# Kernel tuning notes

Hardware: AMD Instinct MI355X
Metric: run time of the kernel (lower is better)

Reference implementation:

```python
import jax, jax.numpy as jnp
import numpy as np

NUM_HEADS = 4
HIDDEN = 128
LN_EPS = 1e-6
NEG_INF = -1e9


def setup_inputs() -> dict:
    key = jax.random.key(0)
    ks = jax.random.split(key, 8)
    B, S, H, NH = 64, 512, HIDDEN, NUM_HEADS
    enc = jax.random.normal(ks[0], (B, S, H), dtype=jnp.float32)
    mask = jax.random.randint(ks[1], (B, 1, S, S), 0, 2, dtype=jnp.int32)
    scale = 1.0 / np.sqrt(H)
    # torch Linear(H, H*NH, bias=False): weight is (H*NH, H); store transposed (H, H*NH)
    Wq = jax.random.normal(ks[2], (H, H * NH), dtype=jnp.float32) * scale
    Wk = jax.random.normal(ks[3], (H, H * NH), dtype=jnp.float32) * scale
    Wv = jax.random.normal(ks[4], (H, H * NH), dtype=jnp.float32) * scale
    Wo = jax.random.normal(ks[5], (H * NH, H), dtype=jnp.float32) * (1.0 / np.sqrt(H * NH))
    gamma = jnp.ones((H,), dtype=jnp.float32)
    beta = jnp.zeros((H,), dtype=jnp.float32)
    return {"enc": enc, "mask": mask, "Wq": Wq, "Wk": Wk, "Wv": Wv, "Wo": Wo, "gamma": gamma, "beta": beta}


def reference(enc, mask, Wq, Wk, Wv, Wo, gamma, beta):
    B, S, H = enc.shape
    NH = NUM_HEADS
    # projections -> (B, NH, S, H): each head has head_dim == hidden_units
    Q = (enc @ Wq).reshape(B, S, NH, H).transpose(0, 2, 1, 3)
    K = (enc @ Wk).reshape(B, S, NH, H).transpose(0, 2, 1, 3)
    V = (enc @ Wv).reshape(B, S, NH, H).transpose(0, 2, 1, 3)
    # scaled dot-product attention with mask (non-flash: full score matrix)
    scores = jnp.einsum('bhqd,bhkd->bhqk', Q, K) / jnp.sqrt(jnp.float32(H))
    scores = jnp.where(mask == 0, jnp.float32(NEG_INF), scores)
    attn = jax.nn.softmax(scores, axis=-1)  # dropout = identity in eval mode
    ctx = jnp.einsum('bhqk,bhkd->bhqd', attn, V)  # (B, NH, S, H)
    ctx = ctx.transpose(0, 2, 1, 3).reshape(B, S, NH * H)
    out = ctx @ Wo + enc  # dropout identity, residual add
    # LayerNorm over last dim
    mu = jnp.mean(out, axis=-1, keepdims=True)
    var = jnp.var(out, axis=-1, keepdims=True)
    return gamma * (out - mu) / jnp.sqrt(var + LN_EPS) + beta
```

## Files before the change

kernel.cpp:

```cpp
#include <hip/hip_runtime.h>
#include <stdint.h>

#define BATCH 64
#define SLEN 512
#define HID 128
#define NHEAD 4
#define DPROJ 512
#define MTOT (BATCH * SLEN)
#define SCALE 0.08838834764831845f

using short8 = __attribute__((ext_vector_type(8))) short;
using f32x4  = __attribute__((ext_vector_type(4))) float;
using u32x4  = __attribute__((ext_vector_type(4))) unsigned int;
using u32x2  = __attribute__((ext_vector_type(2))) unsigned int;
using us4    = __attribute__((ext_vector_type(4))) unsigned short;

__device__ __forceinline__ unsigned short f2bf(float f) {
  unsigned int u = __float_as_uint(f);
  u += 0x7fffu + ((u >> 16) & 1u);
  return (unsigned short)(u >> 16);
}

__global__ __launch_bounds__(256) void prep_kernel(
    const float* __restrict__ Wq,
    const float* __restrict__ Wk,
    const float* __restrict__ Wv,
    const float* __restrict__ Wo,
    const float* __restrict__ enc,
    const int* __restrict__ mask,
    unsigned short* __restrict__ WT,
    unsigned short* __restrict__ WoT,
    unsigned short* __restrict__ encb,
    unsigned int* __restrict__ mbits)
{
  if (blockIdx.x < 1024) {
    int idx = blockIdx.x * 256 + threadIdx.x;
    int z = idx >> 16;
    int i = idx & 65535;
    if (z < 3) {
      const float* W = (z == 0) ? Wq : (z == 1) ? Wk : Wv;
      float scale = (z == 0) ? SCALE : 1.0f;
      int k = i >> 9;
      int n = i & 511;
      WT[(size_t)z * 65536 + (size_t)n * 128 + k] = f2bf(W[i] * scale);
    } else {
      int k = i >> 7;
      int n = i & 127;
      WoT[(size_t)n * 512 + k] = f2bf(Wo[i]);
    }
  } else if (blockIdx.x < 3072) {
    size_t tid = (size_t)(blockIdx.x - 1024) * 256 + threadIdx.x;
    const float* s = enc + tid * 8;
    f32x4 a0 = *(const f32x4*)(s);
    f32x4 a1 = *(const f32x4*)(s + 4);
    short8 v;
    #pragma unroll
    for (int j = 0; j < 4; ++j) v[j] = (short)f2bf(a0[j]);
    #pragma unroll
    for (int j = 0; j < 4; ++j) v[4 + j] = (short)f2bf(a1[j]);
    *(short8*)(encb + tid * 8) = v;
  } else {
    const int l = threadIdx.x & 63;
    size_t wavebase = (size_t)(blockIdx.x - 3072) * 1024 + (threadIdx.x >> 6) * 256;
    unsigned long long b0 = __ballot(mask[wavebase + 0 * 64 + l] != 0);
    unsigned long long b1 = __ballot(mask[wavebase + 1 * 64 + l] != 0);
    unsigned long long b2 = __ballot(mask[wavebase + 2 * 64 + l] != 0);
    unsigned long long b3 = __ballot(mask[wavebase + 3 * 64 + l] != 0);
    if (l < 4) {
      unsigned long long v = (l & 2) ? ((l & 1) ? b3 : b2) : ((l & 1) ? b1 : b0);
      *(unsigned long long*)(mbits + (wavebase >> 5) + l * 2) = v;
    }
  }
}

__global__ __launch_bounds__(256) void qkv_kernel(
    const unsigned short* __restrict__ encb,
    const unsigned short* __restrict__ WT,
    unsigned short* __restrict__ Qh,
    unsigned short* __restrict__ Kh,
    unsigned short* __restrict__ Vt)
{
  const int nt = blockIdx.x;
  const int mt = blockIdx.y;
  const int t = threadIdx.x;
  const int lane = t & 63;
  const int w = t >> 6;
  const int quad = lane >> 4;
  const int l16 = lane & 15;

  __shared__ __align__(16) unsigned short Ald[128 * 136];
  __shared__ __align__(16) unsigned short Bld[128 * 136];

  const int m0 = mt * 128, n0 = nt * 128;
  const int wm = (w >> 1) * 64, wn = (w & 1) * 64;

  #pragma unroll
  for (int i = 0; i < 8; ++i) {
    int idx = i * 256 + t;
    int row = idx >> 4;
    int col = (idx & 15) << 3;
    *(u32x4*)(Ald + row * 136 + col) =
        *(const u32x4*)(encb + (size_t)(m0 + row) * HID + col);
  }

  for (int z = 0; z < 3; ++z) {
    __syncthreads();
    const unsigned short* Wz = WT + (size_t)z * DPROJ * HID;
    #pragma unroll
    for (int i = 0; i < 8; ++i) {
      int idx = i * 256 + t;
      int row = idx >> 4;
      int col = (idx & 15) << 3;
      *(u32x4*)(Bld + row * 136 + col) =
          *(const u32x4*)(Wz + (size_t)(n0 + row) * HID + col);
    }
    __syncthreads();

    f32x4 acc[4][4];
    #pragma unroll
    for (int mi = 0; mi < 4; ++mi)
      #pragma unroll
      for (int ni = 0; ni < 4; ++ni)
        acc[mi][ni] = f32x4{0.f, 0.f, 0.f, 0.f};

    #pragma unroll
    for (int kk = 0; kk < 4; ++kk) {
      short8 a[4], bb[4];
      #pragma unroll
      for (int mi = 0; mi < 4; ++mi)
        a[mi] = *(const short8*)(Ald + (wm + mi * 16 + l16) * 136 + kk * 32 + quad * 8);
      #pragma unroll
      for (int ni = 0; ni < 4; ++ni)
        bb[ni] = *(const short8*)(Bld + (wn + ni * 16 + l16) * 136 + kk * 32 + quad * 8);
      if (z < 2) {
        #pragma unroll
        for (int mi = 0; mi < 4; ++mi)
          #pragma unroll
          for (int ni = 0; ni < 4; ++ni)
            acc[mi][ni] = __builtin_amdgcn_mfma_f32_16x16x32_bf16(bb[ni], a[mi], acc[mi][ni], 0, 0, 0);
      } else {
        #pragma unroll
        for (int mi = 0; mi < 4; ++mi)
          #pragma unroll
          for (int ni = 0; ni < 4; ++ni)
            acc[mi][ni] = __builtin_amdgcn_mfma_f32_16x16x32_bf16(a[mi], bb[ni], acc[mi][ni], 0, 0, 0);
      }
    }

    if (z < 2) {
      unsigned short* outz = ((z == 0) ? Qh : Kh) + (size_t)nt * MTOT * HID;
      #pragma unroll
      for (int mi = 0; mi < 4; ++mi)
        #pragma unroll
        for (int ni = 0; ni < 4; ++ni) {
          int m = m0 + wm + mi * 16 + l16;
          int dbase = wn + ni * 16 + quad * 4;
          us4 pk;
          #pragma unroll
          for (int r = 0; r < 4; ++r) pk[r] = f2bf(acc[mi][ni][r]);
          *(us4*)(outz + (size_t)m * HID + dbase) = pk;
        }
    } else {
      #pragma unroll
      for (int mi = 0; mi < 4; ++mi)
        #pragma unroll
        for (int ni = 0; ni < 4; ++ni) {
          int row0 = m0 + wm + mi * 16 + quad * 4;
          int b = row0 >> 9, s = row0 & 511;
          int d = wn + ni * 16 + l16;
          us4 pk;
          #pragma unroll
          for (int r = 0; r < 4; ++r) pk[r] = f2bf(acc[mi][ni][r]);
          *(us4*)(Vt + ((size_t)(nt * BATCH + b) * HID + d) * SLEN + s) = pk;
        }
    }
  }
}

__global__ __launch_bounds__(512, 4) void attn_kernel(
    const unsigned short* __restrict__ Qh,
    const unsigned short* __restrict__ Kh,
    const unsigned short* __restrict__ Vt,
    const unsigned int* __restrict__ mbits,
    unsigned short* __restrict__ ctx)
{
  const int lin = blockIdx.x;
  const int work = (lin & 7) * 128 + (lin >> 3);
  const int qt = work & 3;
  const int h  = (work >> 2) & 3;
  const int b  = work >> 4;

  const int t = threadIdx.x;
  const int lane = t & 63;
  const int w = t >> 6;
  const int quad = lane >> 4;
  const int l16 = lane & 15;

  __shared__ __align__(16) unsigned short Kld[64 * 136];
  __shared__ __align__(16) unsigned short Vtld[128 * 72];
  __shared__ __align__(16) unsigned short Pld[128 * 64];

  const int q0 = qt * 128;
  const size_t rowbase = (size_t)b * SLEN;
  const unsigned short* kbase0 = Kh + ((size_t)h * MTOT + rowbase) * HID;
  const unsigned short* vbase  = Vt + (size_t)(h * BATCH + b) * HID * SLEN;
  const unsigned int* mrow = mbits + (size_t)b * SLEN * 16;

  const int k_key = t >> 4, k_col = (t & 15) << 3;
  const int v_d   = t >> 3, v_cc  = (t & 7) << 3;

  short8 qa[4];
  {
    const unsigned short* qbase =
        Qh + ((size_t)h * MTOT + rowbase + q0 + w * 16 + l16) * HID + quad * 8;
    #pragma unroll
    for (int kk = 0; kk < 4; ++kk)
      qa[kk] = *(const short8*)(qbase + kk * 32);
  }

  short8 ones;
  #pragma unroll
  for (int j = 0; j < 8; ++j) ones[j] = (short)0x3F80;

  f32x4 oc[8], oc9;
  #pragma unroll
  for (int nd = 0; nd < 8; ++nd) oc[nd] = f32x4{0.f, 0.f, 0.f, 0.f};
  oc9 = f32x4{0.f, 0.f, 0.f, 0.f};

  u32x4 kreg[2], vreg[2];
  #pragma unroll
  for (int i = 0; i < 2; ++i) {
    kreg[i] = *(const u32x4*)(kbase0 + (size_t)(k_key + i * 32) * HID + k_col);
    vreg[i] = *(const u32x4*)(vbase + (size_t)(v_d + i * 64) * SLEN + v_cc);
  }

  for (int c0 = 0; c0 < SLEN; c0 += 64) {
    if (c0) __syncthreads();
    #pragma unroll
    for (int i = 0; i < 2; ++i) {
      *(u32x4*)(Kld + (k_key + i * 32) * 136 + k_col) = kreg[i];
      *(u32x4*)(Vtld + (v_d + i * 64) * 72 + v_cc) = vreg[i];
    }
    __syncthreads();
    if (c0 + 64 < SLEN) {
      #pragma unroll
      for (int i = 0; i < 2; ++i) {
        kreg[i] = *(const u32x4*)(kbase0 + (size_t)(c0 + 64 + k_key + i * 32) * HID + k_col);
        vreg[i] = *(const u32x4*)(vbase + (size_t)(v_d + i * 64) * SLEN + c0 + 64 + v_cc);
      }
    }

    u32x2 mw[4];
    #pragma unroll
    for (int r = 0; r < 4; ++r) {
      int qrow = q0 + w * 16 + quad * 4 + r;
      mw[r] = *(const u32x2*)(mrow + (size_t)qrow * 16 + (c0 >> 5));
    }

    f32x4 sc[4];
    #pragma unroll
    for (int ni = 0; ni < 4; ++ni) sc[ni] = f32x4{0.f, 0.f, 0.f, 0.f};
    #pragma unroll
    for (int kk = 0; kk < 4; ++kk) {
      #pragma unroll
      for (int ni = 0; ni < 4; ++ni) {
        short8 bb = *(const short8*)(Kld + (ni * 16 + l16) * 136 + kk * 32 + quad * 8);
        sc[ni] = __builtin_amdgcn_mfma_f32_16x16x32_bf16(qa[kk], bb, sc[ni], 0, 0, 0);
      }
    }

    #pragma unroll
    for (int ni = 0; ni < 4; ++ni) {
      int bit = (ni & 1) * 16 + l16;
      #pragma unroll
      for (int r = 0; r < 4; ++r) {
        unsigned wsel = (ni < 2) ? mw[r][0] : mw[r][1];
        float e = __expf(sc[ni][r]);
        float p = ((wsel >> bit) & 1u) ? e : 0.f;
        int rowp = w * 16 + quad * 4 + r;
        int cg = (ni * 2 + (l16 >> 3)) ^ (rowp & 7);
        Pld[rowp * 64 + cg * 8 + (l16 & 7)] = f2bf(p);
      }
    }
    __threadfence_block();

    #pragma unroll
    for (int kb = 0; kb < 2; ++kb) {
      int rowr = w * 16 + l16;
      int cg = (kb * 4 + quad) ^ (l16 & 7);
      short8 a = *(const short8*)(Pld + rowr * 64 + cg * 8);
      #pragma unroll
      for (int nd = 0; nd < 8; ++nd) {
        short8 bv = *(const short8*)(Vtld + (nd * 16 + l16) * 72 + kb * 32 + quad * 8);
        oc[nd] = __builtin_amdgcn_mfma_f32_16x16x32_bf16(bv, a, oc[nd], 0, 0, 0);
      }
      oc9 = __builtin_amdgcn_mfma_f32_16x16x32_bf16(ones, a, oc9, 0, 0, 0);
    }
  }

  float rcp = 1.0f / oc9[0];
  int qrow = q0 + w * 16 + l16;
  unsigned short* crow = ctx + (rowbase + qrow) * DPROJ + h * HID;
  #pragma unroll
  for (int nd = 0; nd < 8; ++nd) {
    us4 pk;
    #pragma unroll
    for (int r = 0; r < 4; ++r) pk[r] = f2bf(oc[nd][r] * rcp);
    *(us4*)(crow + nd * 16 + quad * 4) = pk;
  }
}

__global__ __launch_bounds__(256, 4) void oproj_ln_kernel(
    const unsigned short* __restrict__ ctx,
    const unsigned short* __restrict__ WoT,
    const float* __restrict__ enc,
    const float* __restrict__ gamma,
    const float* __restrict__ beta,
    float* __restrict__ out)
{
  const int m0 = blockIdx.x * 64;
  const int t = threadIdx.x;
  const int lane = t & 63;
  const int w = t >> 6;
  const int quad = lane >> 4;
  const int l16 = lane & 15;

  __shared__ __align__(16) unsigned short Actx[64 * 72];
  __shared__ __align__(16) unsigned short Bw[128 * 72];

  f32x4 acc[8];
  #pragma unroll
  for (int ni = 0; ni < 8; ++ni) acc[ni] = f32x4{0.f, 0.f, 0.f, 0.f};

  for (int kc = 0; kc < DPROJ; kc += 64) {
    __syncthreads();
    #pragma unroll
    for (int i = 0; i < 2; ++i) {
      int idx = i * 256 + t;
      int row = idx >> 3;
      int col = (idx & 7) << 3;
      *(u32x4*)(Actx + row * 72 + col) =
          *(const u32x4*)(ctx + (size_t)(m0 + row) * DPROJ + kc + col);
    }
    #pragma unroll
    for (int i = 0; i < 4; ++i) {
      int idx = i * 256 + t;
      int row = idx >> 3;
      int col = (idx & 7) << 3;
      *(u32x4*)(Bw + row * 72 + col) =
          *(const u32x4*)(WoT + (size_t)row * DPROJ + kc + col);
    }
    __syncthreads();
    #pragma unroll
    for (int kk = 0; kk < 2; ++kk) {
      short8 a = *(const short8*)(Actx + (w * 16 + l16) * 72 + kk * 32 + quad * 8);
      #pragma unroll
      for (int ni = 0; ni < 8; ++ni) {
        short8 bb = *(const short8*)(Bw + (ni * 16 + l16) * 72 + kk * 32 + quad * 8);
        acc[ni] = __builtin_amdgcn_mfma_f32_16x16x32_bf16(a, bb, acc[ni], 0, 0, 0);
      }
    }
  }

  float g[8], be[8];
  #pragma unroll
  for (int ni = 0; ni < 8; ++ni) {
    g[ni] = gamma[ni * 16 + l16];
    be[ni] = beta[ni * 16 + l16];
  }

  float val[8][4];
  #pragma unroll
  for (int r = 0; r < 4; ++r) {
    int m = m0 + w * 16 + quad * 4 + r;
    const float* erow = enc + (size_t)m * HID;
    float s = 0.f, s2 = 0.f;
    #pragma unroll
    for (int ni = 0; ni < 8; ++ni) {
      float v = acc[ni][r] + erow[ni * 16 + l16];
      val[ni][r] = v;
      s += v;
      s2 += v * v;
    }
    #pragma unroll
    for (int off = 1; off < 16; off <<= 1) {
      s  += __shfl_xor(s, off, 64);
      s2 += __shfl_xor(s2, off, 64);
    }
    float mean = s * (1.f / 128.f);
    float var = s2 * (1.f / 128.f) - mean * mean;
    float rstd = rsqrtf(var + 1e-6f);
    float* orow = out + (size_t)m * HID;
    #pragma unroll
    for (int ni = 0; ni < 8; ++ni)
      orow[ni * 16 + l16] = g[ni] * (val[ni][r] - mean) * rstd + be[ni];
  }
}

extern "C" void kernel_launch(void* const* d_in, const int* in_sizes, int n_in,
                              void* d_out, int out_size, void* d_ws, size_t ws_size,
                              hipStream_t stream) {
  const float* enc   = (const float*)d_in[0];
  const int*   mask  = (const int*)d_in[1];
  const float* Wq    = (const float*)d_in[2];
  const float* Wk    = (const float*)d_in[3];
  const float* Wv    = (const float*)d_in[4];
  const float* Wo    = (const float*)d_in[5];
  const float* gamma = (const float*)d_in[6];
  const float* beta  = (const float*)d_in[7];
  float* out = (float*)d_out;

  unsigned short* WT  = (unsigned short*)d_ws;
  unsigned short* WoT = WT + (size_t)3 * DPROJ * HID;
  unsigned short* Qh  = WoT + (size_t)HID * DPROJ;
  unsigned short* Kh  = Qh + (size_t)NHEAD * MTOT * HID;
  unsigned short* Vt  = Kh + (size_t)NHEAD * MTOT * HID;
  unsigned short* ctx = Vt + (size_t)NHEAD * MTOT * HID;
  unsigned short* encb = ctx + (size_t)MTOT * DPROJ;
  unsigned int* mbits = (unsigned int*)(encb + (size_t)MTOT * HID * 2);

  prep_kernel<<<19456, 256, 0, stream>>>(Wq, Wk, Wv, Wo, enc, mask, WT, WoT, encb, mbits);
  qkv_kernel<<<dim3(4, 256), 256, 0, stream>>>(encb, WT, Qh, Kh, Vt);
  attn_kernel<<<1024, 512, 0, stream>>>(Qh, Kh, Vt, mbits, ctx);
  oproj_ln_kernel<<<MTOT / 64, 256, 0, stream>>>(ctx, WoT, enc, gamma, beta, out);
}
```

Measured before the change: 246.5 us.

## Drop LDS staging in attention; read K/V from global, shuffle P in registers

The attention kernel no longer stages K, V and P through shared memory. Each wave now loads its K and V fragments straight from global memory (relying on the cache), and the P matrix is rearranged into MFMA operand layout with cross-lane shuffles. This removes the block-wide barriers. Blocks shrink to 256 threads covering 64 query rows, doubling the grid, and log2(e) is folded into the Q weight scale so exp2f can replace __expf. The trade-off is much more redundant global and L2 traffic for K/V, since every wave re-reads the same tiles.

```diff
diff --git a/kernel.cpp b/kernel.cpp
--- a/kernel.cpp
+++ b/kernel.cpp
@@ -8,6 +8,7 @@
 #define DPROJ 512
 #define MTOT (BATCH * SLEN)
 #define SCALE 0.08838834764831845f
+#define LOG2E 1.4426950408889634f
 
 using short8 = __attribute__((ext_vector_type(8))) short;
 using f32x4  = __attribute__((ext_vector_type(4))) float;
@@ -39,7 +40,7 @@
     int i = idx & 65535;
     if (z < 3) {
       const float* W = (z == 0) ? Wq : (z == 1) ? Wk : Wv;
-      float scale = (z == 0) ? SCALE : 1.0f;
+      float scale = (z == 0) ? (SCALE * LOG2E) : 1.0f;
       int k = i >> 9;
       int n = i & 511;
       WT[(size_t)z * 65536 + (size_t)n * 128 + k] = f2bf(W[i] * scale);
@@ -177,7 +178,7 @@
   }
 }
 
-__global__ __launch_bounds__(512, 4) void attn_kernel(
+__global__ __launch_bounds__(256, 4) void attn_kernel(
     const unsigned short* __restrict__ Qh,
     const unsigned short* __restrict__ Kh,
     const unsigned short* __restrict__ Vt,
@@ -185,10 +186,10 @@
     unsigned short* __restrict__ ctx)
 {
   const int lin = blockIdx.x;
-  const int work = (lin & 7) * 128 + (lin >> 3);
-  const int qt = work & 3;
-  const int h  = (work >> 2) & 3;
-  const int b  = work >> 4;
+  const int work = (lin & 7) * 256 + (lin >> 3);
+  const int qt = work & 7;
+  const int hb = work >> 3;
+  const int h = hb & 3, b = hb >> 2;
 
   const int t = threadIdx.x;
   const int lane = t & 63;
@@ -196,23 +197,17 @@
   const int quad = lane >> 4;
   const int l16 = lane & 15;
 
-  __shared__ __align__(16) unsigned short Kld[64 * 136];
-  __shared__ __align__(16) unsigned short Vtld[128 * 72];
-  __shared__ __align__(16) unsigned short Pld[128 * 64];
-
-  const int q0 = qt * 128;
+  const int q0 = qt * 64;
   const size_t rowbase = (size_t)b * SLEN;
-  const unsigned short* kbase0 = Kh + ((size_t)h * MTOT + rowbase) * HID;
-  const unsigned short* vbase  = Vt + (size_t)(h * BATCH + b) * HID * SLEN;
-  const unsigned int* mrow = mbits + (size_t)b * SLEN * 16;
-
-  const int k_key = t >> 4, k_col = (t & 15) << 3;
-  const int v_d   = t >> 3, v_cc  = (t & 7) << 3;
+  const unsigned short* kbase = Kh + ((size_t)h * MTOT + rowbase) * HID;
+  const unsigned short* vbase = Vt + (size_t)(h * BATCH + b) * HID * SLEN;
+  const int qrow = q0 + w * 16 + l16;
+  const unsigned int* mrow = mbits + ((size_t)b * SLEN + qrow) * 16;
 
   short8 qa[4];
   {
     const unsigned short* qbase =
-        Qh + ((size_t)h * MTOT + rowbase + q0 + w * 16 + l16) * HID + quad * 8;
+        Qh + ((size_t)h * MTOT + rowbase + qrow) * HID + quad * 8;
     #pragma unroll
     for (int kk = 0; kk < 4; ++kk)
       qa[kk] = *(const short8*)(qbase + kk * 32);
@@ -227,86 +222,65 @@
   for (int nd = 0; nd < 8; ++nd) oc[nd] = f32x4{0.f, 0.f, 0.f, 0.f};
   oc9 = f32x4{0.f, 0.f, 0.f, 0.f};
 
-  u32x4 kreg[2], vreg[2];
-  #pragma unroll
-  for (int i = 0; i < 2; ++i) {
-    kreg[i] = *(const u32x4*)(kbase0 + (size_t)(k_key + i * 32) * HID + k_col);
-    vreg[i] = *(const u32x4*)(vbase + (size_t)(v_d + i * 64) * SLEN + v_cc);
-  }
+  const int srcA = 2 * (quad & 1) * 16 + l16;
 
   for (int c0 = 0; c0 < SLEN; c0 += 64) {
-    if (c0) __syncthreads();
-    #pragma unroll
-    for (int i = 0; i < 2; ++i) {
-      *(u32x4*)(Kld + (k_key + i * 32) * 136 + k_col) = kreg[i];
-      *(u32x4*)(Vtld + (v_d + i * 64) * 72 + v_cc) = vreg[i];
-    }
-    __syncthreads();
-    if (c0 + 64 < SLEN) {
-      #pragma unroll
-      for (int i = 0; i < 2; ++i) {
-        kreg[i] = *(const u32x4*)(kbase0 + (size_t)(c0 + 64 + k_key + i * 32) * HID + k_col);
-        vreg[i] = *(const u32x4*)(vbase + (size_t)(v_d + i * 64) * SLEN + c0 + 64 + v_cc);
+    f32x4 sc[4];
+    #pragma unroll
+    for (int ni = 0; ni < 4; ++ni) sc[ni] = f32x4{0.f, 0.f, 0.f, 0.f};
+    #pragma unroll
+    for (int kk = 0; kk < 4; ++kk) {
+      #pragma unroll
+      for (int ni = 0; ni < 4; ++ni) {
+        short8 bb = *(const short8*)(kbase + (size_t)(c0 + ni * 16 + l16) * HID + kk * 32 + quad * 8);
+        sc[ni] = __builtin_amdgcn_mfma_f32_16x16x32_bf16(bb, qa[kk], sc[ni], 0, 0, 0);
       }
     }
 
-    u32x2 mw[4];
-    #pragma unroll
-    for (int r = 0; r < 4; ++r) {
-      int qrow = q0 + w * 16 + quad * 4 + r;
-      mw[r] = *(const u32x2*)(mrow + (size_t)qrow * 16 + (c0 >> 5));
-    }
-
-    f32x4 sc[4];
-    #pragma unroll
-    for (int ni = 0; ni < 4; ++ni) sc[ni] = f32x4{0.f, 0.f, 0.f, 0.f};
-    #pragma unroll
-    for (int kk = 0; kk < 4; ++kk) {
-      #pragma unroll
-      for (int ni = 0; ni < 4; ++ni) {
-        short8 bb = *(const short8*)(Kld + (ni * 16 + l16) * 136 + kk * 32 + quad * 8);
-        sc[ni] = __builtin_amdgcn_mfma_f32_16x16x32_bf16(qa[kk], bb, sc[ni], 0, 0, 0);
+    u32x2 mw = *(const u32x2*)(mrow + (c0 >> 5));
+    unsigned long long mk = ((unsigned long long)mw[1] << 32) | (unsigned long long)mw[0];
+
+    unsigned long long pk64[4];
+    #pragma unroll
+    for (int ni = 0; ni < 4; ++ni) {
+      us4 pk;
+      #pragma unroll
+      for (int r = 0; r < 4; ++r) {
+        float e = exp2f(sc[ni][r]);
+        float p = ((mk >> (ni * 16 + quad * 4 + r)) & 1ull) ? e : 0.f;
+        pk[r] = f2bf(p);
       }
-    }
-
-    #pragma unroll
-    for (int ni = 0; ni < 4; ++ni) {
-      int bit = (ni & 1) * 16 + l16;
-      #pragma unroll
-      for (int r = 0; r < 4; ++r) {
-        unsigned wsel = (ni < 2) ? mw[r][0] : mw[r][1];
-        float e = __expf(sc[ni][r]);
-        float p = ((wsel >> bit) & 1u) ? e : 0.f;
-        int rowp = w * 16 + quad * 4 + r;
-        int cg = (ni * 2 + (l16 >> 3)) ^ (rowp & 7);
-        Pld[rowp * 64 + cg * 8 + (l16 & 7)] = f2bf(p);
+      pk64[ni] = *(unsigned long long*)&pk;
+    }
+
+    #pragma unroll
+    for (int kb = 0; kb < 2; ++kb) {
+      unsigned long long lo0 = __shfl(pk64[2 * kb + 0], srcA, 64);
+      unsigned long long lo1 = __shfl(pk64[2 * kb + 1], srcA, 64);
+      unsigned long long hi0 = __shfl(pk64[2 * kb + 0], srcA + 16, 64);
+      unsigned long long hi1 = __shfl(pk64[2 * kb + 1], srcA + 16, 64);
+      unsigned long long lo = (quad & 2) ? lo1 : lo0;
+      unsigned long long hi = (quad & 2) ? hi1 : hi0;
+      union { struct { unsigned long long x, y; } u; short8 v; } af;
+      af.u.x = lo; af.u.y = hi;
+      short8 a = af.v;
+      #pragma unroll
+      for (int nd = 0; nd < 8; ++nd) {
+        short8 bv = *(const short8*)(vbase + (size_t)(nd * 16 + l16) * SLEN + c0 + kb * 32 + quad * 8);
+        oc[nd] = __builtin_amdgcn_mfma_f32_16x16x32_bf16(a, bv, oc[nd], 0, 0, 0);
       }
-    }
-    __threadfence_block();
-
-    #pragma unroll
-    for (int kb = 0; kb < 2; ++kb) {
-      int rowr = w * 16 + l16;
-      int cg = (kb * 4 + quad) ^ (l16 & 7);
-      short8 a = *(const short8*)(Pld + rowr * 64 + cg * 8);
-      #pragma unroll
-      for (int nd = 0; nd < 8; ++nd) {
-        short8 bv = *(const short8*)(Vtld + (nd * 16 + l16) * 72 + kb * 32 + quad * 8);
-        oc[nd] = __builtin_amdgcn_mfma_f32_16x16x32_bf16(bv, a, oc[nd], 0, 0, 0);
-      }
-      oc9 = __builtin_amdgcn_mfma_f32_16x16x32_bf16(ones, a, oc9, 0, 0, 0);
-    }
-  }
-
-  float rcp = 1.0f / oc9[0];
-  int qrow = q0 + w * 16 + l16;
-  unsigned short* crow = ctx + (rowbase + qrow) * DPROJ + h * HID;
-  #pragma unroll
-  for (int nd = 0; nd < 8; ++nd) {
-    us4 pk;
-    #pragma unroll
-    for (int r = 0; r < 4; ++r) pk[r] = f2bf(oc[nd][r] * rcp);
-    *(us4*)(crow + nd * 16 + quad * 4) = pk;
+      oc9 = __builtin_amdgcn_mfma_f32_16x16x32_bf16(a, ones, oc9, 0, 0, 0);
+    }
+  }
+
+  #pragma unroll
+  for (int r = 0; r < 4; ++r) {
+    float rcp = 1.0f / oc9[r];
+    int row = q0 + w * 16 + quad * 4 + r;
+    unsigned short* crow = ctx + (rowbase + row) * DPROJ + h * HID;
+    #pragma unroll
+    for (int nd = 0; nd < 8; ++nd)
+      crow[nd * 16 + l16] = f2bf(oc[nd][r] * rcp);
   }
 }
 
@@ -421,6 +395,6 @@
 
   prep_kernel<<<19456, 256, 0, stream>>>(Wq, Wk, Wv, Wo, enc, mask, WT, WoT, encb, mbits);
   qkv_kernel<<<dim3(4, 256), 256, 0, stream>>>(encb, WT, Qh, Kh, Vt);
-  attn_kernel<<<1024, 512, 0, stream>>>(Qh, Kh, Vt, mbits, ctx);
+  attn_kernel<<<2048, 256, 0, stream>>>(Qh, Kh, Vt, mbits, ctx);
   oproj_ln_kernel<<<MTOT / 64, 256, 0, stream>>>(ctx, WoT, enc, gamma, beta, out);
 }
```

After: 413.2 us. 67.6% more time.
